# Kernel optimization log

Measured on AMD Instinct MI355X. Metric: run time of the kernel, lower is better.

Reference implementation:

```python
import jax, jax.numpy as jnp
import numpy as np

DIM = 1024
NUM_HEADS = 16
HEAD_DIM = DIM // NUM_HEADS


def setup_inputs() -> dict:
    key = jax.random.key(0)
    k_x, k_wqkv, k_bqkv, k_wo, k_bo = jax.random.split(key, 5)
    B, N = 2, 2048
    s = 1.0 / np.sqrt(DIM)
    return {
        "x": jax.random.normal(k_x, (B, N, DIM), dtype=jnp.float32),
        "w_qkv": jax.random.uniform(k_wqkv, (DIM, 3 * DIM), jnp.float32, -s, s),
        "b_qkv": jax.random.uniform(k_bqkv, (3 * DIM,), jnp.float32, -s, s),
        "w_out": jax.random.uniform(k_wo, (DIM, DIM), jnp.float32, -s, s),
        "b_out": jax.random.uniform(k_bo, (DIM,), jnp.float32, -s, s),
    }


def reference(x, w_qkv, b_qkv, w_out, b_out):
    B, N, D = x.shape
    H, Hd = NUM_HEADS, HEAD_DIM
    scale = Hd ** -0.5
    qkv = x @ w_qkv + b_qkv                      # [B,N,3D]
    qkv = qkv.reshape(B, N, 3, H, Hd).transpose(2, 0, 3, 1, 4)  # [3,B,H,N,Hd]
    q, k, v = qkv[0], qkv[1], qkv[2]
    scores = jnp.einsum("bhqd,bhkd->bhqk", q, k) * scale
    attn = jax.nn.softmax(scores, axis=-1)
    out = jnp.einsum("bhqk,bhkd->bhqd", attn, v)  # [B,H,N,Hd]
    out = out.transpose(0, 2, 1, 3).reshape(B, N, D)
    return out @ w_out + b_out
```

## Files before the change

kernel.cpp:

```cpp
#include <hip/hip_runtime.h>
#include <stdint.h>

#define D_MODEL 1024
#define NHEADS 16
#define HDIM 64
#define BATCH 2
#define SEQ 2048
#define MTOK (BATCH*SEQ)

typedef unsigned short u16;
typedef __attribute__((ext_vector_type(8))) __bf16 bf16x8;
typedef __attribute__((ext_vector_type(8))) unsigned short u16x8;
typedef __attribute__((ext_vector_type(4))) unsigned short u16x4;
typedef __attribute__((ext_vector_type(4))) float f32x4;
typedef __attribute__((ext_vector_type(16))) float f32x16;
typedef __attribute__((ext_vector_type(2))) unsigned int u32x2;

__device__ __forceinline__ u16 f2bf(float f) {
  union { float f; uint32_t u; } v; v.f = f;
  uint32_t u = v.u;
  u += 0x7fffu + ((u >> 16) & 1u);
  return (u16)(u >> 16);
}

__device__ __forceinline__ u16 f2bf_hw(float f) {
  return __builtin_bit_cast(u16, (__bf16)f);
}

__device__ __forceinline__ unsigned cvtpk(float a, float b) {
  unsigned r;
  asm("v_cvt_pk_bf16_f32 %0, %1, %2" : "=v"(r) : "v"(a), "v"(b));
  return r;
}

__device__ __forceinline__ u32x2 plswap(unsigned a, unsigned b) {
#if __has_builtin(__builtin_amdgcn_permlane32_swap)
  return __builtin_amdgcn_permlane32_swap(a, b, false, false);
#else
  asm("v_permlane32_swap_b32 %0, %1" : "+v"(a), "+v"(b));
  u32x2 r; r.x = a; r.y = b; return r;
#endif
}

__device__ __forceinline__ void async16(u16* lds, const u16* g) {
  __builtin_amdgcn_global_load_lds(
      (__attribute__((address_space(1))) void*)(u16*)g,
      (__attribute__((address_space(3))) void*)lds,
      16, 0, 0);
}

__device__ __forceinline__ void transpose_cast_body(
    const float* __restrict__ in, u16* __restrict__ out, int R, int C,
    int bid, int tid, float (*tile)[33])
{
  int nCB = C >> 5;
  int bc = bid % nCB, br = bid / nCB;
  int r0 = br * 32, c0 = bc * 32;
  int tx = tid & 31, ty = tid >> 5;
#pragma unroll
  for (int i = 0; i < 4; ++i)
    tile[ty + i*8][tx] = in[(size_t)(r0 + ty + i*8) * C + c0 + tx];
  __syncthreads();
#pragma unroll
  for (int i = 0; i < 4; ++i)
    out[(size_t)(c0 + ty + i*8) * R + r0 + tx] = f2bf(tile[tx][ty + i*8]);
}

__global__ __launch_bounds__(256) void prep_kernel(
    const float* __restrict__ x, const float* __restrict__ w_qkv,
    const float* __restrict__ w_out,
    u16* __restrict__ x_bf, u16* __restrict__ wqkv_t, u16* __restrict__ wout_t)
{
  __shared__ float tile[32][33];
  int bid = blockIdx.x, tid = threadIdx.x;
  if (bid < 2048) {
    int i = bid * 256 + tid;
    const float4* p = (const float4*)(x + (size_t)i * 8);
    float4 a = p[0], b = p[1];
    u16x8 r;
    r[0]=f2bf(a.x); r[1]=f2bf(a.y); r[2]=f2bf(a.z); r[3]=f2bf(a.w);
    r[4]=f2bf(b.x); r[5]=f2bf(b.y); r[6]=f2bf(b.z); r[7]=f2bf(b.w);
    *(u16x8*)(x_bf + (size_t)i * 8) = r;
  } else if (bid < 2048 + 3072) {
    transpose_cast_body(w_qkv, wqkv_t, 1024, 3072, bid - 2048, tid, tile);
  } else {
    transpose_cast_body(w_out, wout_t, 1024, 1024, bid - 5120, tid, tile);
  }
}

template <int EPI>
__global__ __launch_bounds__(512, 6) void gemm_bt_kernel(
    const u16* __restrict__ A, const u16* __restrict__ Bt,
    const float* __restrict__ bias,
    float* __restrict__ outF,
    u16* __restrict__ qb, u16* __restrict__ kb, u16* __restrict__ vt,
    int M, int Nn, int K)
{
  __shared__ alignas(16) u16 As[128 * 64];
  __shared__ alignas(16) u16 Bs[128 * 64];

  const int tid = threadIdx.x;
  const int wid = tid >> 6, lane = tid & 63;
  const int col = lane & 15, kg = lane >> 4;
  const int csw = (col & 7) << 3;

  const int nTN = Nn >> 7;
  int bidx = blockIdx.x;
  {
    int cpx = gridDim.x >> 3;
    bidx = (bidx & 7) * cpx + (bidx >> 3);
  }
  const int tile_m = (bidx / nTN) << 7;
  const int tile_n = (bidx % nTN) << 7;
  const int wm = (wid >> 2) << 6;
  const int wn = (wid & 3) << 5;

  f32x4 acc[4][2] = {};

  const int sr = tid >> 3;
  const int sc = (tid & 7) << 3;
  const int ssc = sc ^ ((sr & 7) << 3);

  const int nk = K >> 6;
  for (int kt = 0; kt < nk; ++kt) {
    __syncthreads();
#pragma unroll
    for (int i = 0; i < 2; ++i)
      async16(&As[(i*64 + sr) * 64 + sc],
              A + (size_t)(tile_m + i*64 + sr) * K + kt*64 + ssc);
#pragma unroll
    for (int i = 0; i < 2; ++i)
      async16(&Bs[(i*64 + sr) * 64 + sc],
              Bt + (size_t)(tile_n + i*64 + sr) * K + kt*64 + ssc);
    __syncthreads();

#pragma unroll
    for (int ks = 0; ks < 2; ++ks) {
      bf16x8 af[4], bfv[2];
#pragma unroll
      for (int i = 0; i < 4; ++i)
        af[i] = *(const bf16x8*)&As[(wm + i*16 + col) * 64 + ((ks*32 + kg*8) ^ csw)];
#pragma unroll
      for (int j = 0; j < 2; ++j)
        bfv[j] = *(const bf16x8*)&Bs[(wn + j*16 + col) * 64 + ((ks*32 + kg*8) ^ csw)];
#pragma unroll
      for (int i = 0; i < 4; ++i)
#pragma unroll
        for (int j = 0; j < 2; ++j)
          acc[i][j] = __builtin_amdgcn_mfma_f32_16x16x32_bf16(af[i], bfv[j], acc[i][j], 0, 0, 0);
    }
  }

#pragma unroll
  for (int i = 0; i < 4; ++i) {
#pragma unroll
    for (int jn = 0; jn < 2; ++jn) {
      const int gcol = tile_n + wn + jn*16 + col;
      const float bv = bias[gcol];
      const int grow0 = tile_m + wm + i*16 + kg*4;
      if (EPI == 1) {
#pragma unroll
        for (int j = 0; j < 4; ++j)
          outF[(size_t)(grow0 + j) * Nn + gcol] = acc[i][jn][j] + bv;
      } else {
        const int btok = grow0 >> 11, tok0 = grow0 & 2047;
        const int which = gcol >> 10, f = gcol & 1023;
        const int h = f >> 6, hd = f & 63;
        if (which == 2) {
          u16x4 pk;
#pragma unroll
          for (int j = 0; j < 4; ++j) pk[j] = f2bf(acc[i][jn][j] + bv);
          *(u16x4*)&vt[((size_t)(btok*NHEADS + h) * HDIM + hd) * SEQ + tok0] = pk;
        } else {
#pragma unroll
          for (int j = 0; j < 4; ++j) {
            float val = acc[i][jn][j] + bv;
            size_t dst = ((size_t)(btok*NHEADS + h) * SEQ + tok0 + j) * HDIM + hd;
            if (which == 0) qb[dst] = f2bf(val * 0.18033688f);
            else            kb[dst] = f2bf(val);
          }
        }
      }
    }
  }
}

__global__ __launch_bounds__(256, 2) void attn_kernel(
    const u16* __restrict__ qb, const u16* __restrict__ kb,
    const u16* __restrict__ vt, u16* __restrict__ ao)
{
  __shared__ alignas(16) u16 Ks[128 * 64];
  __shared__ alignas(16) u16 Vs[64 * 128];

  const int tid = threadIdx.x, wid = tid >> 6, lane = tid & 63;
  const int c31 = lane & 31, hi = lane >> 5;
  const int rsw = (lane & 7) << 3;

  int bidx = blockIdx.x;
  bidx = (bidx & 7) * 64 + (bidx >> 3);
  const int bh = bidx >> 4;
  const int qt = bidx & 15;

  const u16* Qh = qb + (size_t)bh * SEQ * HDIM;
  const u16* Kh = kb + (size_t)bh * SEQ * HDIM;
  const u16* Vh = vt + (size_t)bh * SEQ * HDIM;

  const int q0 = qt * 128 + wid * 32;
  bf16x8 qf[4];
#pragma unroll
  for (int kk = 0; kk < 4; ++kk)
    qf[kk] = *(const bf16x8*)(Qh + (size_t)(q0 + c31) * HDIM + kk*16 + hi*8);

  float l_run = 0.f;
  f32x16 o[2] = {};

  const int krow = tid >> 1, kc = (tid & 1) << 5, ksw = (krow & 7) << 3;
  const int vrow = tid >> 2, vc = (tid & 3) << 5, vsw = (vrow & 7) << 3;

  u16x8 kreg[4], vreg[4];
#define LOAD_TILES(t)                                                               \
  {                                                                                 \
    _Pragma("unroll")                                                               \
    for (int i = 0; i < 4; ++i)                                                     \
      kreg[i] = *(const u16x8*)(Kh + (size_t)((t)*128 + krow) * HDIM + kc + i*8);   \
    _Pragma("unroll")                                                               \
    for (int i = 0; i < 4; ++i)                                                     \
      vreg[i] = *(const u16x8*)(Vh + (size_t)vrow * SEQ + (t)*128 + vc + i*8);      \
  }

  LOAD_TILES(0);

  for (int t = 0; t < 16; ++t) {
    __syncthreads();
#pragma unroll
    for (int i = 0; i < 4; ++i)
      *(u16x8*)&Ks[krow * 64 + ((kc + i*8) ^ ksw)] = kreg[i];
#pragma unroll
    for (int i = 0; i < 4; ++i)
      *(u16x8*)&Vs[vrow * 128 + ((vc + i*8) ^ vsw)] = vreg[i];
    __syncthreads();
    if (t < 15) LOAD_TILES(t + 1);

    f32x16 s[4] = {};
#pragma unroll
    for (int kk = 0; kk < 4; ++kk) {
#pragma unroll
      for (int nt = 0; nt < 4; ++nt) {
        bf16x8 kf = *(const bf16x8*)&Ks[(nt*32 + c31) * 64 + ((kk*16 + hi*8) ^ rsw)];
        s[nt] = __builtin_amdgcn_mfma_f32_32x32x16_bf16(kf, qf[kk], s[nt], 0, 0, 0);
      }
    }

#pragma unroll
    for (int nt = 0; nt < 4; ++nt) {
      float sum = 0.f;
#pragma unroll
      for (int r = 0; r < 16; ++r) {
        s[nt][r] = __builtin_amdgcn_exp2f(s[nt][r]);
        sum += s[nt][r];
      }
      l_run += sum;
    }

#pragma unroll
    for (int kk = 0; kk < 8; ++kk) {
      const int nt = kk >> 1, rb = (kk & 1) * 8;
      unsigned A0 = cvtpk(s[nt][rb+0], s[nt][rb+1]);
      unsigned A1 = cvtpk(s[nt][rb+2], s[nt][rb+3]);
      unsigned B0 = cvtpk(s[nt][rb+4], s[nt][rb+5]);
      unsigned B1 = cvtpk(s[nt][rb+6], s[nt][rb+7]);
      u32x2 p0 = plswap(A0, B0);
      u32x2 p1 = plswap(A1, B1);
      union { unsigned w[4]; bf16x8 v; } pf;
      pf.w[0] = p0.x; pf.w[1] = p1.x; pf.w[2] = p0.y; pf.w[3] = p1.y;
#pragma unroll
      for (int dt = 0; dt < 2; ++dt) {
        bf16x8 vf = *(const bf16x8*)&Vs[(dt*32 + c31) * 128 + ((kk*16 + hi*8) ^ rsw)];
        o[dt] = __builtin_amdgcn_mfma_f32_32x32x16_bf16(vf, pf.v, o[dt], 0, 0, 0);
      }
    }
  }

  const int bb = bh >> 4, h = bh & 15;
  {
    float l = l_run + __shfl_xor(l_run, 32);
    float inv = 1.0f / l;
    const int nrow = q0 + c31;
#pragma unroll
    for (int dt = 0; dt < 2; ++dt) {
#pragma unroll
      for (int tq = 0; tq < 4; ++tq) {
        u16x4 pk;
#pragma unroll
        for (int j = 0; j < 4; ++j) pk[j] = f2bf(o[dt][tq*4 + j] * inv);
        int feat = h*64 + dt*32 + tq*8 + hi*4;
        *(u16x4*)&ao[(size_t)(bb * SEQ + nrow) * D_MODEL + feat] = pk;
      }
    }
  }
#undef LOAD_TILES
}

extern "C" void kernel_launch(void* const* d_in, const int* in_sizes, int n_in,
                              void* d_out, int out_size, void* d_ws, size_t ws_size,
                              hipStream_t stream)
{
  const float* x     = (const float*)d_in[0];
  const float* w_qkv = (const float*)d_in[1];
  const float* b_qkv = (const float*)d_in[2];
  const float* w_out = (const float*)d_in[3];
  const float* b_out = (const float*)d_in[4];
  float* out = (float*)d_out;
  (void)in_sizes; (void)n_in; (void)out_size; (void)ws_size;

  char* ws = (char*)d_ws;
  u16* x_bf   = (u16*)(ws);
  u16* wqkv_t = (u16*)(ws + (size_t)( 8 << 20));
  u16* wout_t = (u16*)(ws + (size_t)(14 << 20));
  u16* qb     = (u16*)(ws + (size_t)(16 << 20));
  u16* kb     = (u16*)(ws + (size_t)(24 << 20));
  u16* vt     = (u16*)(ws + (size_t)(32 << 20));
  u16* ao     = (u16*)(ws + (size_t)(40 << 20));

  prep_kernel<<<2048 + 3072 + 1024, 256, 0, stream>>>(x, w_qkv, w_out, x_bf, wqkv_t, wout_t);

  gemm_bt_kernel<0><<<(MTOK/128)*(3072/128), 512, 0, stream>>>(
      x_bf, wqkv_t, b_qkv, nullptr, qb, kb, vt, MTOK, 3072, 1024);

  attn_kernel<<<32*16, 256, 0, stream>>>(qb, kb, vt, ao);

  gemm_bt_kernel<1><<<(MTOK/128)*(1024/128), 512, 0, stream>>>(
      ao, wout_t, b_out, out, nullptr, nullptr, nullptr, MTOK, 1024, 1024);
}
```

Baseline: 109.7 us.

## Split attention KV range across two blocks and add combine kernel

Each attention block now handles half the key/value sequence, so the grid doubles from 512 to 1024 blocks. Each block writes partial normalized outputs in bf16 plus its row sums, and a new combine kernel merges the two halves weighted by their sums. Launch bounds rise to 4 waves per SIMD to fit more blocks per CU. The aim is more parallelism to fill the 256 CUs, at the cost of an extra launch, extra global traffic for partial outputs, and an extra bf16 rounding step. The merge relies on softmax with no running max, so unnormalized sums combine exactly.

```diff
diff --git a/kernel.cpp b/kernel.cpp
--- a/kernel.cpp
+++ b/kernel.cpp
@@ -23,8 +23,9 @@
   return (u16)(u >> 16);
 }
 
-__device__ __forceinline__ u16 f2bf_hw(float f) {
-  return __builtin_bit_cast(u16, (__bf16)f);
+__device__ __forceinline__ float bf2f(u16 u) {
+  union { uint32_t u; float f; } v; v.u = ((uint32_t)u) << 16;
+  return v.f;
 }
 
 __device__ __forceinline__ unsigned cvtpk(float a, float b) {
@@ -185,9 +186,9 @@
   }
 }
 
-__global__ __launch_bounds__(256, 2) void attn_kernel(
+__global__ __launch_bounds__(256, 4) void attn_kernel(
     const u16* __restrict__ qb, const u16* __restrict__ kb,
-    const u16* __restrict__ vt, u16* __restrict__ ao)
+    const u16* __restrict__ vt, u16* __restrict__ onb, float* __restrict__ lp)
 {
   __shared__ alignas(16) u16 Ks[128 * 64];
   __shared__ alignas(16) u16 Vs[64 * 128];
@@ -197,9 +198,10 @@
   const int rsw = (lane & 7) << 3;
 
   int bidx = blockIdx.x;
-  bidx = (bidx & 7) * 64 + (bidx >> 3);
-  const int bh = bidx >> 4;
-  const int qt = bidx & 15;
+  bidx = (bidx & 7) * 128 + (bidx >> 3);
+  const int bh   = bidx >> 5;
+  const int qt   = (bidx >> 1) & 15;
+  const int half = bidx & 1;
 
   const u16* Qh = qb + (size_t)bh * SEQ * HDIM;
   const u16* Kh = kb + (size_t)bh * SEQ * HDIM;
@@ -228,9 +230,10 @@
       vreg[i] = *(const u16x8*)(Vh + (size_t)vrow * SEQ + (t)*128 + vc + i*8);      \
   }
 
-  LOAD_TILES(0);
-
-  for (int t = 0; t < 16; ++t) {
+  const int t0 = half * 8;
+  LOAD_TILES(t0);
+
+  for (int t = t0; t < t0 + 8; ++t) {
     __syncthreads();
 #pragma unroll
     for (int i = 0; i < 4; ++i)
@@ -239,7 +242,7 @@
     for (int i = 0; i < 4; ++i)
       *(u16x8*)&Vs[vrow * 128 + ((vc + i*8) ^ vsw)] = vreg[i];
     __syncthreads();
-    if (t < 15) LOAD_TILES(t + 1);
+    if (t < t0 + 7) LOAD_TILES(t + 1);
 
     f32x16 s[4] = {};
 #pragma unroll
@@ -286,6 +289,7 @@
     float l = l_run + __shfl_xor(l_run, 32);
     float inv = 1.0f / l;
     const int nrow = q0 + c31;
+    u16* onH = onb + (size_t)half * MTOK * D_MODEL;
 #pragma unroll
     for (int dt = 0; dt < 2; ++dt) {
 #pragma unroll
@@ -294,11 +298,36 @@
 #pragma unroll
         for (int j = 0; j < 4; ++j) pk[j] = f2bf(o[dt][tq*4 + j] * inv);
         int feat = h*64 + dt*32 + tq*8 + hi*4;
-        *(u16x4*)&ao[(size_t)(bb * SEQ + nrow) * D_MODEL + feat] = pk;
-      }
-    }
+        *(u16x4*)&onH[(size_t)(bb * SEQ + nrow) * D_MODEL + feat] = pk;
+      }
+    }
+    if (hi == 0)
+      lp[((size_t)half*32 + bh) * SEQ + nrow] = l;
   }
 #undef LOAD_TILES
+}
+
+__global__ __launch_bounds__(256) void combine_kernel(
+    const u16* __restrict__ onb, const float* __restrict__ lp,
+    u16* __restrict__ ao)
+{
+  int idx = blockIdx.x * 256 + threadIdx.x;
+  int tok = idx >> 7;
+  int f8  = (idx & 127) << 3;
+  int h   = f8 >> 6;
+  int bh  = ((tok >> 11) << 4) | h;
+  int q   = tok & 2047;
+  float l0 = lp[(size_t)bh * SEQ + q];
+  float l1 = lp[(size_t)(32 + bh) * SEQ + q];
+  float inv = 1.0f / (l0 + l1);
+  float w0 = l0 * inv, w1 = l1 * inv;
+  u16x8 o0 = *(const u16x8*)&onb[(size_t)tok * D_MODEL + f8];
+  u16x8 o1 = *(const u16x8*)&onb[(size_t)MTOK * D_MODEL + (size_t)tok * D_MODEL + f8];
+  u16x8 r;
+#pragma unroll
+  for (int j = 0; j < 8; ++j)
+    r[j] = f2bf(w0 * bf2f(o0[j]) + w1 * bf2f(o1[j]));
+  *(u16x8*)&ao[(size_t)tok * D_MODEL + f8] = r;
 }
 
 extern "C" void kernel_launch(void* const* d_in, const int* in_sizes, int n_in,
@@ -314,20 +343,24 @@
   (void)in_sizes; (void)n_in; (void)out_size; (void)ws_size;
 
   char* ws = (char*)d_ws;
-  u16* x_bf   = (u16*)(ws);
-  u16* wqkv_t = (u16*)(ws + (size_t)( 8 << 20));
-  u16* wout_t = (u16*)(ws + (size_t)(14 << 20));
-  u16* qb     = (u16*)(ws + (size_t)(16 << 20));
-  u16* kb     = (u16*)(ws + (size_t)(24 << 20));
-  u16* vt     = (u16*)(ws + (size_t)(32 << 20));
-  u16* ao     = (u16*)(ws + (size_t)(40 << 20));
+  u16*   x_bf   = (u16*)(ws);
+  u16*   wqkv_t = (u16*)(ws + (size_t)( 8 << 20));
+  u16*   wout_t = (u16*)(ws + (size_t)(14 << 20));
+  u16*   qb     = (u16*)(ws + (size_t)(16 << 20));
+  u16*   kb     = (u16*)(ws + (size_t)(24 << 20));
+  u16*   vt     = (u16*)(ws + (size_t)(32 << 20));
+  u16*   ao     = (u16*)(ws + (size_t)(40 << 20));
+  u16*   onb    = (u16*)(ws + (size_t)(48 << 20));
+  float* lpart  = (float*)(ws + (size_t)(64 << 20));
 
   prep_kernel<<<2048 + 3072 + 1024, 256, 0, stream>>>(x, w_qkv, w_out, x_bf, wqkv_t, wout_t);
 
   gemm_bt_kernel<0><<<(MTOK/128)*(3072/128), 512, 0, stream>>>(
       x_bf, wqkv_t, b_qkv, nullptr, qb, kb, vt, MTOK, 3072, 1024);
 
-  attn_kernel<<<32*16, 256, 0, stream>>>(qb, kb, vt, ao);
+  attn_kernel<<<32*16*2, 256, 0, stream>>>(qb, kb, vt, onb, lpart);
+
+  combine_kernel<<<(MTOK*D_MODEL/8)/256, 256, 0, stream>>>(onb, lpart, ao);
 
   gemm_bt_kernel<1><<<(MTOK/128)*(1024/128), 512, 0, stream>>>(
       ao, wout_t, b_out, out, nullptr, nullptr, nullptr, MTOK, 1024, 1024);
```

Result: slower. 247.2 us (+125.3%).

## Shrink attention blocks to 64 queries and load K/V tiles via async LDS copies

Applied to the files above, without the earlier changes.

The attention kernel now runs two waves per block covering 64 query rows, launched as twice as many blocks. K/V tiles are no longer prefetched through registers; instead wave 0 issues async global-to-LDS copies for K and wave 1 for V, with the XOR swizzle folded into the global source address. This cuts register pressure and the LDS store instructions, and the extra blocks may help occupancy. In exchange, the register-based prefetch of the next tile is gone, so loads no longer overlap compute within a block, and each K/V tile is re-read by twice as many blocks.

```diff
diff --git a/kernel.cpp b/kernel.cpp
--- a/kernel.cpp
+++ b/kernel.cpp
@@ -21,10 +21,6 @@
   uint32_t u = v.u;
   u += 0x7fffu + ((u >> 16) & 1u);
   return (u16)(u >> 16);
-}
-
-__device__ __forceinline__ u16 f2bf_hw(float f) {
-  return __builtin_bit_cast(u16, (__bf16)f);
 }
 
 __device__ __forceinline__ unsigned cvtpk(float a, float b) {
@@ -185,7 +181,7 @@
   }
 }
 
-__global__ __launch_bounds__(256, 2) void attn_kernel(
+__global__ __launch_bounds__(128, 2) void attn_kernel(
     const u16* __restrict__ qb, const u16* __restrict__ kb,
     const u16* __restrict__ vt, u16* __restrict__ ao)
 {
@@ -197,15 +193,15 @@
   const int rsw = (lane & 7) << 3;
 
   int bidx = blockIdx.x;
-  bidx = (bidx & 7) * 64 + (bidx >> 3);
-  const int bh = bidx >> 4;
-  const int qt = bidx & 15;
+  bidx = (bidx & 7) * 128 + (bidx >> 3);
+  const int bh = bidx >> 5;
+  const int qt = bidx & 31;
 
   const u16* Qh = qb + (size_t)bh * SEQ * HDIM;
   const u16* Kh = kb + (size_t)bh * SEQ * HDIM;
   const u16* Vh = vt + (size_t)bh * SEQ * HDIM;
 
-  const int q0 = qt * 128 + wid * 32;
+  const int q0 = qt * 64 + wid * 32;
   bf16x8 qf[4];
 #pragma unroll
   for (int kk = 0; kk < 4; ++kk)
@@ -214,32 +210,27 @@
   float l_run = 0.f;
   f32x16 o[2] = {};
 
-  const int krow = tid >> 1, kc = (tid & 1) << 5, ksw = (krow & 7) << 3;
-  const int vrow = tid >> 2, vc = (tid & 3) << 5, vsw = (vrow & 7) << 3;
-
-  u16x8 kreg[4], vreg[4];
-#define LOAD_TILES(t)                                                               \
-  {                                                                                 \
-    _Pragma("unroll")                                                               \
-    for (int i = 0; i < 4; ++i)                                                     \
-      kreg[i] = *(const u16x8*)(Kh + (size_t)((t)*128 + krow) * HDIM + kc + i*8);   \
-    _Pragma("unroll")                                                               \
-    for (int i = 0; i < 4; ++i)                                                     \
-      vreg[i] = *(const u16x8*)(Vh + (size_t)vrow * SEQ + (t)*128 + vc + i*8);      \
-  }
-
-  LOAD_TILES(0);
+  const int krow_l = lane >> 3, kg_l = lane & 7;
+  const int kgp = kg_l ^ krow_l;
+  const int vrow_l = lane >> 4, vg_l = lane & 15;
 
   for (int t = 0; t < 16; ++t) {
     __syncthreads();
-#pragma unroll
-    for (int i = 0; i < 4; ++i)
-      *(u16x8*)&Ks[krow * 64 + ((kc + i*8) ^ ksw)] = kreg[i];
-#pragma unroll
-    for (int i = 0; i < 4; ++i)
-      *(u16x8*)&Vs[vrow * 128 + ((vc + i*8) ^ vsw)] = vreg[i];
+    if (wid == 0) {
+#pragma unroll
+      for (int c = 0; c < 16; ++c)
+        async16(&Ks[c*512 + lane*8],
+                Kh + (size_t)(t*128 + c*8 + krow_l) * HDIM + kgp*8);
+    } else {
+#pragma unroll
+      for (int c = 0; c < 16; ++c) {
+        int row = c*4 + vrow_l;
+        int gp = vg_l ^ (row & 7);
+        async16(&Vs[c*512 + lane*8],
+                Vh + (size_t)row * SEQ + t*128 + gp*8);
+      }
+    }
     __syncthreads();
-    if (t < 15) LOAD_TILES(t + 1);
 
     f32x16 s[4] = {};
 #pragma unroll
@@ -298,7 +289,6 @@
       }
     }
   }
-#undef LOAD_TILES
 }
 
 extern "C" void kernel_launch(void* const* d_in, const int* in_sizes, int n_in,
@@ -327,7 +317,7 @@
   gemm_bt_kernel<0><<<(MTOK/128)*(3072/128), 512, 0, stream>>>(
       x_bf, wqkv_t, b_qkv, nullptr, qb, kb, vt, MTOK, 3072, 1024);
 
-  attn_kernel<<<32*16, 256, 0, stream>>>(qb, kb, vt, ao);
+  attn_kernel<<<32*32, 128, 0, stream>>>(qb, kb, vt, ao);
 
   gemm_bt_kernel<1><<<(MTOK/128)*(1024/128), 512, 0, stream>>>(
       ao, wout_t, b_out, out, nullptr, nullptr, nullptr, MTOK, 1024, 1024);
```

Result: slower. 112.7 us (+2.7%).
